# Performance work log

Measured on AMD Instinct MI355X. Metric: run time of the kernel, lower is better.

Reference implementation:

```python
import jax, jax.numpy as jnp
import numpy as np

HEADS = 4
DIM_HEAD = 32
NUM_GROUPS = 8
EPS = 1e-5


def setup_inputs() -> dict:
    key = jax.random.key(0)
    k1, k2, k3, k4 = jax.random.split(key, 4)
    dim = 256
    hidden = HEADS * DIM_HEAD  # 128
    x = jax.random.normal(k1, (4, dim, 64, 64), dtype=jnp.float32)
    # 1x1 convs stored as plain matrices [out_ch, in_ch]
    w_qkv = jax.random.normal(k2, (hidden * 3, dim), dtype=jnp.float32) * (1.0 / np.sqrt(dim))
    w_out = jax.random.normal(k3, (dim, hidden), dtype=jnp.float32) * (1.0 / np.sqrt(hidden))
    b_out = jnp.zeros((dim,), dtype=jnp.float32)
    gamma = jnp.ones((dim,), dtype=jnp.float32)
    beta = jnp.zeros((dim,), dtype=jnp.float32)
    return {"x": x, "w_qkv": w_qkv, "w_out": w_out, "b_out": b_out, "gamma": gamma, "beta": beta}


def group_norm(x, gamma, beta):
    b, c, h, w = x.shape
    xg = x.reshape(b, NUM_GROUPS, c // NUM_GROUPS, h, w)
    mean = xg.mean(axis=(2, 3, 4), keepdims=True)
    var = xg.var(axis=(2, 3, 4), keepdims=True)
    xg = (xg - mean) * jax.lax.rsqrt(var + EPS)
    x = xg.reshape(b, c, h, w)
    return x * gamma[None, :, None, None] + beta[None, :, None, None]


def reference(x, w_qkv, w_out, b_out, gamma, beta):
    b, c, h, w = x.shape
    n = h * w
    scale = DIM_HEAD ** -0.5
    xn = group_norm(x, gamma, beta)  # [b,c,h,w]
    # 1x1 conv QKV: [b, 3*hidden, n]
    qkv = jnp.einsum('oc,bchw->bohw', w_qkv, xn).reshape(b, 3 * HEADS * DIM_HEAD, n)
    q, k, v = jnp.split(qkv, 3, axis=1)
    # -> [b, heads, dim_head, n]
    q = q.reshape(b, HEADS, DIM_HEAD, n) * scale
    k = k.reshape(b, HEADS, DIM_HEAD, n)
    v = v.reshape(b, HEADS, DIM_HEAD, n)
    sim = jnp.einsum('bhdi,bhdj->bhij', q, k)  # [b,heads,n,n]
    sim = sim - jax.lax.stop_gradient(jnp.max(sim, axis=-1, keepdims=True))
    attn = jax.nn.softmax(sim, axis=-1)
    out = jnp.einsum('bhij,bhdj->bhid', attn, v)  # [b,heads,n,dim_head]
    # 'b h (x y) d -> b (h d) x y'
    out = out.transpose(0, 1, 3, 2).reshape(b, HEADS * DIM_HEAD, h, w)
    out = jnp.einsum('oc,bchw->bohw', w_out, out) + b_out[None, :, None, None]
    return out
```

## Files before the change

### kernel.cpp

```cpp
#include <hip/hip_runtime.h>
#include <hip/hip_bf16.h>

typedef float f32x4 __attribute__((ext_vector_type(4)));
typedef short s16x8 __attribute__((ext_vector_type(8)));

__device__ __forceinline__ short f2bf(float f){
  union { float f; unsigned u; } v; v.f = f;
  unsigned u = v.u;
  u += 0x7fffu + ((u >> 16) & 1u);
  return (short)(u >> 16);
}

__device__ __forceinline__ f32x4 mfma16(s16x8 a, s16x8 b, f32x4 c){
  return __builtin_amdgcn_mfma_f32_16x16x32_bf16(a, b, c, 0, 0, 0);
}

__device__ __forceinline__ float fexp2(float x){
#if __has_builtin(__builtin_amdgcn_exp2f)
  return __builtin_amdgcn_exp2f(x);
#else
  float r; asm("v_exp_f32 %0, %1" : "=v"(r) : "v"(x)); return r;
#endif
}

__device__ __forceinline__ unsigned cvtpk(float lo, float hi){
  unsigned r; asm("v_cvt_pk_bf16_f32 %0, %1, %2" : "=v"(r) : "v"(lo), "v"(hi));
  return r;
}

__global__ __launch_bounds__(256) void gn_stats_cvt_k(const float* __restrict__ x,
                                                      const float* __restrict__ wq,
                                                      const float* __restrict__ wo,
                                                      float* __restrict__ part,
                                                      short* __restrict__ wq_bf,
                                                      short* __restrict__ wo_bf){
  int bx = blockIdx.x;
  if (bx >= 1024){
    int i = (bx - 1024)*256 + threadIdx.x;
    if (i < 384*256) wq_bf[i] = f2bf(wq[i]);
    if (i < 256*128) wo_bf[i] = f2bf(wo[i]);
    return;
  }
  const float4* base = ((const float4*)x) + (size_t)bx * 1024;
  float s = 0.f, s2 = 0.f;
  #pragma unroll
  for (int i = threadIdx.x; i < 1024; i += 256){
    float4 v = base[i];
    s  += v.x + v.y + v.z + v.w;
    s2 += v.x*v.x + v.y*v.y + v.z*v.z + v.w*v.w;
  }
  #pragma unroll
  for (int off = 32; off; off >>= 1){ s += __shfl_down(s, off); s2 += __shfl_down(s2, off); }
  __shared__ float ls[8];
  int wid = threadIdx.x >> 6;
  if ((threadIdx.x & 63) == 0){ ls[wid] = s; ls[4 + wid] = s2; }
  __syncthreads();
  if (threadIdx.x == 0){
    part[bx*2]     = ls[0]+ls[1]+ls[2]+ls[3];
    part[bx*2 + 1] = ls[4]+ls[5]+ls[6]+ls[7];
  }
}

__global__ __launch_bounds__(256) void gn_apply_k(const float* __restrict__ x,
                                                  const float* __restrict__ gamma,
                                                  const float* __restrict__ beta,
                                                  const float* __restrict__ part,
                                                  short* __restrict__ xnt){
  __shared__ float lds[64][65];
  int b = blockIdx.z, cg = blockIdx.y, pt = blockIdx.x;
  int t = threadIdx.x;
  int ci = t >> 6, pj = t & 63;
  int p0 = pt * 64;
  float mean[2], rs[2];
  #pragma unroll
  for (int gi = 0; gi < 2; ++gi){
    int bg = b*8 + cg*2 + gi;
    float S = 0.f, S2 = 0.f;
    #pragma unroll
    for (int sl = 0; sl < 32; ++sl){ S += part[(bg*32+sl)*2]; S2 += part[(bg*32+sl)*2+1]; }
    float m = S * (1.f/131072.f);
    mean[gi] = m;
    rs[gi] = rsqrtf(S2 * (1.f/131072.f) - m*m + 1e-5f);
  }
  #pragma unroll
  for (int r = 0; r < 16; ++r){
    int cl = r*4 + ci;
    int c = cg*64 + cl;
    float v = x[((size_t)(b*256 + c))*4096 + p0 + pj];
    int gl = cl >> 5;
    v = (v - mean[gl]) * rs[gl] * gamma[c] + beta[c];
    lds[cl][pj] = v;
  }
  __syncthreads();
  #pragma unroll
  for (int r = 0; r < 16; ++r){
    int pl = r*4 + ci;
    int cl = pj;
    xnt[((size_t)(b*4096 + p0 + pl))*256 + cg*64 + cl] = f2bf(lds[cl][pl]);
  }
}

__global__ __launch_bounds__(256) void qkv_gemm_k(const short* __restrict__ wq_bf,
                                                  const short* __restrict__ xnt,
                                                  short* __restrict__ q,
                                                  short* __restrict__ k,
                                                  short* __restrict__ vt){
  int b = blockIdx.z;
  int obase = blockIdx.y * 64;
  int pbase = blockIdx.x * 64;
  int t = threadIdx.x;
  int w = t >> 6, l = t & 63;
  int l15 = l & 15, g = l >> 4;
  int orow = obase + w*16 + l15;
  const s16x8* wrow = (const s16x8*)(wq_bf + (size_t)orow * 256);
  s16x8 af[8];
  #pragma unroll
  for (int kk = 0; kk < 8; ++kk) af[kk] = wrow[kk*4 + g];
  const float QSC = 0.17677669529663687f * 1.4426950408889634f;
  #pragma unroll
  for (int pt = 0; pt < 4; ++pt){
    int p = pbase + pt*16 + l15;
    const s16x8* xr = (const s16x8*)(xnt + ((size_t)b*4096 + p) * 256);
    f32x4 acc = {0.f,0.f,0.f,0.f};
    #pragma unroll
    for (int kk = 0; kk < 8; ++kk) acc = mfma16(af[kk], xr[kk*4 + g], acc);
    int pp = p & 31;
    int pos = ((pp>>2)&3)*8 + ((pp>>4)&1)*4 + (pp&3);
    int pperm = (p & ~31) | pos;
    #pragma unroll
    for (int e = 0; e < 4; ++e){
      int og = obase + w*16 + 4*g + e;
      float v = acc[e];
      int sec = og >> 7;
      int oh = og & 127;
      int h = oh >> 5, d = oh & 31;
      size_t qk_idx = (((size_t)b*4 + h)*4096 + p)*32 + d;
      if (sec == 0)      q[qk_idx] = f2bf(v * QSC);
      else if (sec == 1) k[qk_idx] = f2bf(v);
      else vt[(((size_t)b*4 + h)*32 + d)*4096 + pperm] = f2bf(v);
    }
  }
}

__global__ __launch_bounds__(256, 4) void flash_k(const short* __restrict__ q,
                                                  const short* __restrict__ k,
                                                  const short* __restrict__ vt,
                                                  short* __restrict__ at){
  __shared__ short ldsS[4*4096];
  __shared__ float sums[4][64];
  int bid = blockIdx.x;
  int lin = (bid & 7)*128 + (bid >> 3);
  int bh = lin >> 6;
  int rt  = lin & 63;
  int b = bh >> 2, h = bh & 3;
  int blkrow = rt * 64;
  int t = threadIdx.x;
  int w = t >> 6, l = t & 63, l15 = l & 15, g = l >> 4;

  const short* qb = q  + (size_t)bh * 4096 * 32;
  const short* kb = k  + (size_t)bh * 4096 * 32;
  const short* vb = vt + (size_t)bh * 32 * 4096;

  s16x8 qf[4];
  #pragma unroll
  for (int it = 0; it < 4; ++it)
    qf[it] = *(const s16x8*)(qb + (size_t)(blkrow + it*16 + l15)*32 + 8*g);

  int wbase = w * 4096;
  int rk = wbase + l15*40 + g*8;
  int rv = wbase + 1280 + l15*40 + g*8;
  int row = l >> 1, hi = (l & 1) * 16;
  int wk = wbase + row*40 + hi;
  int wv = wbase + 1280 + row*40 + hi;

  const short* kq = kb + (size_t)w*32768 + l*16;
  const short* vq = vb + (size_t)row*4096 + w*1024 + hi;

  f32x4 o[4][2];
  float lsum[4];
  #pragma unroll
  for (int it = 0; it < 4; ++it){
    o[it][0] = (f32x4){0.f,0.f,0.f,0.f};
    o[it][1] = (f32x4){0.f,0.f,0.f,0.f};
    lsum[it] = 0.f;
  }
  const f32x4 zero = {0.f,0.f,0.f,0.f};

  s16x8 ka0, ka1, va0, va1;

#define FENCE() asm volatile("" ::: "memory")
#define KVLOAD() do{ ka0 = *(const s16x8*)kq; ka1 = *(const s16x8*)(kq + 8); kq += 1024; \
                     va0 = *(const s16x8*)vq; va1 = *(const s16x8*)(vq + 8); vq += 32; }while(0)
#define KVSTORE() do{ *(s16x8*)&ldsS[wk] = ka0; *(s16x8*)&ldsS[wk + 8] = ka1; \
                      *(s16x8*)&ldsS[wv] = va0; *(s16x8*)&ldsS[wv + 8] = va1; }while(0)
#define COMPUTE() do{ \
    s16x8 kf0 = *(const s16x8*)&ldsS[rk]; \
    s16x8 kf1 = *(const s16x8*)&ldsS[rk + 640]; \
    s16x8 vf0 = *(const s16x8*)&ldsS[rv]; \
    s16x8 vf1 = *(const s16x8*)&ldsS[rv + 640]; \
    _Pragma("unroll") \
    for (int it = 0; it < 4; ++it){ \
      f32x4 s0 = mfma16(kf0, qf[it], zero); \
      f32x4 s1 = mfma16(kf1, qf[it], zero); \
      float p0=fexp2(s0[0]), p1=fexp2(s0[1]), p2=fexp2(s0[2]), p3=fexp2(s0[3]); \
      float p4=fexp2(s1[0]), p5=fexp2(s1[1]), p6=fexp2(s1[2]), p7=fexp2(s1[3]); \
      lsum[it] += ((p0+p1)+(p2+p3)) + ((p4+p5)+(p6+p7)); \
      union { s16x8 v; unsigned u[4]; } pf; \
      pf.u[0] = cvtpk(p0,p1); pf.u[1] = cvtpk(p2,p3); \
      pf.u[2] = cvtpk(p4,p5); pf.u[3] = cvtpk(p6,p7); \
      o[it][0] = mfma16(pf.v, vf0, o[it][0]); \
      o[it][1] = mfma16(pf.v, vf1, o[it][1]); \
    } \
  }while(0)

  KVLOAD();
  KVSTORE();
  FENCE();
  for (int tt = 0; tt < 31; ++tt){
    KVLOAD();
    COMPUTE();
    FENCE();
    KVSTORE();
    FENCE();
  }
  COMPUTE();
#undef KVLOAD
#undef KVSTORE
#undef COMPUTE

  #pragma unroll
  for (int it = 0; it < 4; ++it){
    lsum[it] += __shfl_xor(lsum[it], 16);
    lsum[it] += __shfl_xor(lsum[it], 32);
  }

  FENCE();
  float* cmb = (float*)ldsS;
  #pragma unroll
  for (int it = 0; it < 4; ++it){
    #pragma unroll
    for (int e = 0; e < 4; ++e){
      int r = it*16 + 4*g + e;
      cmb[w*2048 + r*32 + l15]      = o[it][0][e];
      cmb[w*2048 + r*32 + 16 + l15] = o[it][1][e];
    }
    if (l < 16) sums[w][it*16 + l15] = lsum[it];
  }
  __syncthreads();

  int r = t >> 2, d0 = (t & 3) * 8;
  float den = (sums[0][r] + sums[1][r]) + (sums[2][r] + sums[3][r]);
  float inv = 1.f / den;
  s16x8 outv;
  #pragma unroll
  for (int kk = 0; kk < 8; ++kk){
    float num = (cmb[r*32 + d0 + kk] + cmb[2048 + r*32 + d0 + kk])
              + (cmb[4096 + r*32 + d0 + kk] + cmb[6144 + r*32 + d0 + kk]);
    outv[kk] = f2bf(num * inv);
  }
  *(s16x8*)(at + ((size_t)b*4096 + blkrow + r)*128 + h*32 + d0) = outv;
}

__global__ __launch_bounds__(256) void out_gemm_k(const short* __restrict__ wo_bf,
                                                  const short* __restrict__ at,
                                                  const float* __restrict__ b_out,
                                                  float* __restrict__ out){
  int b = blockIdx.z;
  int obase = blockIdx.y * 64;
  int pbase = blockIdx.x * 64;
  int t = threadIdx.x, w = t >> 6, l = t & 63, l15 = l & 15, g = l >> 4;
  int orow = obase + w*16 + l15;
  const s16x8* wrow = (const s16x8*)(wo_bf + (size_t)orow * 128);
  s16x8 af[4];
  #pragma unroll
  for (int kk = 0; kk < 4; ++kk) af[kk] = wrow[kk*4 + g];
  #pragma unroll
  for (int pt = 0; pt < 4; ++pt){
    int p = pbase + pt*16 + l15;
    const s16x8* xr = (const s16x8*)(at + ((size_t)b*4096 + p) * 128);
    f32x4 acc = {0.f,0.f,0.f,0.f};
    #pragma unroll
    for (int kk = 0; kk < 4; ++kk) acc = mfma16(af[kk], xr[kk*4 + g], acc);
    #pragma unroll
    for (int e = 0; e < 4; ++e){
      int og = obase + w*16 + 4*g + e;
      out[((size_t)b*256 + og)*4096 + p] = acc[e] + b_out[og];
    }
  }
}

extern "C" void kernel_launch(void* const* d_in, const int* in_sizes, int n_in,
                              void* d_out, int out_size, void* d_ws, size_t ws_size,
                              hipStream_t stream){
  const float* x     = (const float*)d_in[0];
  const float* w_qkv = (const float*)d_in[1];
  const float* w_out = (const float*)d_in[2];
  const float* b_out = (const float*)d_in[3];
  const float* gamma = (const float*)d_in[4];
  const float* beta  = (const float*)d_in[5];
  float* out = (float*)d_out;

  char* ws = (char*)d_ws;
  short* wq_bf = (short*)(ws);
  short* wo_bf = (short*)(ws + 196608);
  short* xnt   = (short*)(ws + 264192);
  short* qbuf  = (short*)(ws + 8652800);
  short* kbuf  = (short*)(ws + 12847104);
  short* vtbuf = (short*)(ws + 17041408);
  short* atbuf = (short*)(ws + 21235712);
  float* part  = (float*)(ws + 21235712);

  hipLaunchKernelGGL(gn_stats_cvt_k, dim3(1408), dim3(256), 0, stream, x, w_qkv, w_out, part, wq_bf, wo_bf);
  hipLaunchKernelGGL(gn_apply_k, dim3(64,4,4),   dim3(256), 0, stream, x, gamma, beta, part, xnt);
  hipLaunchKernelGGL(qkv_gemm_k, dim3(64,6,4),   dim3(256), 0, stream, wq_bf, xnt, qbuf, kbuf, vtbuf);
  hipLaunchKernelGGL(flash_k,    dim3(1024),     dim3(256), 0, stream, qbuf, kbuf, vtbuf, atbuf);
  hipLaunchKernelGGL(out_gemm_k, dim3(64,4,4),   dim3(256), 0, stream, wo_bf, atbuf, b_out, out);
}
```

Before: 110.4 us.

## Fuse group-norm apply into QKV GEMM and slim flash epilogue LDS usage

Merges the group-norm apply kernel with the QKV projection. Each block normalizes a 32-pixel tile of all 256 channels into LDS as bf16 and then runs the MFMA GEMM for all 384 output rows. This removes the xnt intermediate write and read to global memory and drops one kernel launch. The flash epilogue now combines per-wave partial outputs in two half-passes, each wave using its own padded LDS region, which drops the separate sums array. The fused kernel has only 512 blocks, makes narrower 32-float strided reads of x, and reloads weight fragments per output tile.

```diff
diff --git a/kernel.cpp b/kernel.cpp
--- a/kernel.cpp
+++ b/kernel.cpp
@@ -61,83 +61,84 @@
   }
 }
 
-__global__ __launch_bounds__(256) void gn_apply_k(const float* __restrict__ x,
-                                                  const float* __restrict__ gamma,
-                                                  const float* __restrict__ beta,
-                                                  const float* __restrict__ part,
-                                                  short* __restrict__ xnt){
-  __shared__ float lds[64][65];
-  int b = blockIdx.z, cg = blockIdx.y, pt = blockIdx.x;
+__global__ __launch_bounds__(256) void gn_qkv_k(const float* __restrict__ x,
+                                                const float* __restrict__ part,
+                                                const float* __restrict__ gamma,
+                                                const float* __restrict__ beta,
+                                                const short* __restrict__ wq_bf,
+                                                short* __restrict__ q,
+                                                short* __restrict__ k,
+                                                short* __restrict__ vt){
+  __shared__ float stg[64][33];
+  __shared__ short xl[32*264];
+  __shared__ float mstat[16];
+  int b = blockIdx.y;
+  int p0 = blockIdx.x * 32;
   int t = threadIdx.x;
-  int ci = t >> 6, pj = t & 63;
-  int p0 = pt * 64;
-  float mean[2], rs[2];
-  #pragma unroll
-  for (int gi = 0; gi < 2; ++gi){
-    int bg = b*8 + cg*2 + gi;
-    float S = 0.f, S2 = 0.f;
-    #pragma unroll
-    for (int sl = 0; sl < 32; ++sl){ S += part[(bg*32+sl)*2]; S2 += part[(bg*32+sl)*2+1]; }
-    float m = S * (1.f/131072.f);
-    mean[gi] = m;
-    rs[gi] = rsqrtf(S2 * (1.f/131072.f) - m*m + 1e-5f);
-  }
-  #pragma unroll
-  for (int r = 0; r < 16; ++r){
-    int cl = r*4 + ci;
-    int c = cg*64 + cl;
-    float v = x[((size_t)(b*256 + c))*4096 + p0 + pj];
-    int gl = cl >> 5;
-    v = (v - mean[gl]) * rs[gl] * gamma[c] + beta[c];
-    lds[cl][pj] = v;
-  }
-  __syncthreads();
-  #pragma unroll
-  for (int r = 0; r < 16; ++r){
-    int pl = r*4 + ci;
-    int cl = pj;
-    xnt[((size_t)(b*4096 + p0 + pl))*256 + cg*64 + cl] = f2bf(lds[cl][pl]);
-  }
-}
-
-__global__ __launch_bounds__(256) void qkv_gemm_k(const short* __restrict__ wq_bf,
-                                                  const short* __restrict__ xnt,
-                                                  short* __restrict__ q,
-                                                  short* __restrict__ k,
-                                                  short* __restrict__ vt){
-  int b = blockIdx.z;
-  int obase = blockIdx.y * 64;
-  int pbase = blockIdx.x * 64;
-  int t = threadIdx.x;
-  int w = t >> 6, l = t & 63;
-  int l15 = l & 15, g = l >> 4;
-  int orow = obase + w*16 + l15;
-  const s16x8* wrow = (const s16x8*)(wq_bf + (size_t)orow * 256);
-  s16x8 af[8];
-  #pragma unroll
-  for (int kk = 0; kk < 8; ++kk) af[kk] = wrow[kk*4 + g];
+  {
+    int gi = t >> 5, sl = t & 31;
+    float S  = part[((b*8+gi)*32 + sl)*2];
+    float S2 = part[((b*8+gi)*32 + sl)*2 + 1];
+    #pragma unroll
+    for (int m = 16; m; m >>= 1){ S += __shfl_xor(S, m); S2 += __shfl_xor(S2, m); }
+    if (sl == 0){
+      float mn = S * (1.f/131072.f);
+      mstat[gi]   = mn;
+      mstat[8+gi] = rsqrtf(S2 * (1.f/131072.f) - mn*mn + 1e-5f);
+    }
+  }
+  __syncthreads();
+  int pj = t & 31, ci8 = t >> 5;
+  for (int cc = 0; cc < 4; ++cc){
+    #pragma unroll
+    for (int r = 0; r < 8; ++r){
+      int cl = r*8 + ci8;
+      int c = cc*64 + cl;
+      float v = x[((size_t)(b*256 + c))*4096 + p0 + pj];
+      int gl = c >> 5;
+      v = (v - mstat[gl]) * mstat[8+gl] * gamma[c] + beta[c];
+      stg[cl][pj] = v;
+    }
+    __syncthreads();
+    {
+      s16x8 pack;
+      #pragma unroll
+      for (int i = 0; i < 8; ++i) pack[i] = f2bf(stg[ci8*8 + i][pj]);
+      *(s16x8*)&xl[pj*264 + cc*64 + ci8*8] = pack;
+    }
+    __syncthreads();
+  }
+  int w = t >> 6, l = t & 63, l15 = l & 15, g = l >> 4;
   const float QSC = 0.17677669529663687f * 1.4426950408889634f;
   #pragma unroll
-  for (int pt = 0; pt < 4; ++pt){
-    int p = pbase + pt*16 + l15;
-    const s16x8* xr = (const s16x8*)(xnt + ((size_t)b*4096 + p) * 256);
-    f32x4 acc = {0.f,0.f,0.f,0.f};
-    #pragma unroll
-    for (int kk = 0; kk < 8; ++kk) acc = mfma16(af[kk], xr[kk*4 + g], acc);
-    int pp = p & 31;
-    int pos = ((pp>>2)&3)*8 + ((pp>>4)&1)*4 + (pp&3);
-    int pperm = (p & ~31) | pos;
-    #pragma unroll
-    for (int e = 0; e < 4; ++e){
-      int og = obase + w*16 + 4*g + e;
-      float v = acc[e];
-      int sec = og >> 7;
-      int oh = og & 127;
-      int h = oh >> 5, d = oh & 31;
-      size_t qk_idx = (((size_t)b*4 + h)*4096 + p)*32 + d;
-      if (sec == 0)      q[qk_idx] = f2bf(v * QSC);
-      else if (sec == 1) k[qk_idx] = f2bf(v);
-      else vt[(((size_t)b*4 + h)*32 + d)*4096 + pperm] = f2bf(v);
+  for (int ot = 0; ot < 6; ++ot){
+    int orow = w*96 + ot*16 + l15;
+    const s16x8* wrow = (const s16x8*)(wq_bf + (size_t)orow * 256);
+    s16x8 af[8];
+    #pragma unroll
+    for (int kk = 0; kk < 8; ++kk) af[kk] = wrow[kk*4 + g];
+    #pragma unroll
+    for (int pt = 0; pt < 2; ++pt){
+      f32x4 acc = {0.f,0.f,0.f,0.f};
+      #pragma unroll
+      for (int kk = 0; kk < 8; ++kk)
+        acc = mfma16(af[kk], *(const s16x8*)&xl[(pt*16+l15)*264 + kk*32 + g*8], acc);
+      int p = p0 + pt*16 + l15;
+      int pp = p & 31;
+      int pos = ((pp>>2)&3)*8 + ((pp>>4)&1)*4 + (pp&3);
+      int pperm = (p & ~31) | pos;
+      #pragma unroll
+      for (int e = 0; e < 4; ++e){
+        int og = w*96 + ot*16 + 4*g + e;
+        float v = acc[e];
+        int sec = og >> 7;
+        int oh = og & 127;
+        int h = oh >> 5, d = oh & 31;
+        size_t qk_idx = (((size_t)b*4 + h)*4096 + p)*32 + d;
+        if (sec == 0)      q[qk_idx] = f2bf(v * QSC);
+        else if (sec == 1) k[qk_idx] = f2bf(v);
+        else vt[(((size_t)b*4 + h)*32 + d)*4096 + pperm] = f2bf(v);
+      }
     }
   }
 }
@@ -147,7 +148,6 @@
                                                   const short* __restrict__ vt,
                                                   short* __restrict__ at){
   __shared__ short ldsS[4*4096];
-  __shared__ float sums[4][64];
   int bid = blockIdx.x;
   int lin = (bid & 7)*128 + (bid >> 3);
   int bh = lin >> 6;
@@ -235,30 +235,53 @@
   }
 
   FENCE();
-  float* cmb = (float*)ldsS;
+  float* cw = (float*)&ldsS[wbase];
   #pragma unroll
   for (int it = 0; it < 4; ++it){
     #pragma unroll
     for (int e = 0; e < 4; ++e){
       int r = it*16 + 4*g + e;
-      cmb[w*2048 + r*32 + l15]      = o[it][0][e];
-      cmb[w*2048 + r*32 + 16 + l15] = o[it][1][e];
-    }
-    if (l < 16) sums[w][it*16 + l15] = lsum[it];
-  }
-  __syncthreads();
-
-  int r = t >> 2, d0 = (t & 3) * 8;
-  float den = (sums[0][r] + sums[1][r]) + (sums[2][r] + sums[3][r]);
+      cw[r*17 + l15] = o[it][0][e];
+    }
+    if (l < 16) cw[1088 + it*16 + l15] = lsum[it];
+  }
+  __syncthreads();
+  int rr = t >> 2, a = t & 3;
+  size_t rowbase = ((size_t)b*4096 + blkrow + rr)*128 + h*32;
+  float den = 0.f, n0 = 0.f, n1 = 0.f, n2 = 0.f, n3 = 0.f;
+  #pragma unroll
+  for (int w2 = 0; w2 < 4; ++w2){
+    const float* cr = (const float*)&ldsS[w2*4096];
+    den += cr[1088 + rr];
+    n0 += cr[rr*17 + a*4];
+    n1 += cr[rr*17 + a*4 + 1];
+    n2 += cr[rr*17 + a*4 + 2];
+    n3 += cr[rr*17 + a*4 + 3];
+  }
   float inv = 1.f / den;
-  s16x8 outv;
-  #pragma unroll
-  for (int kk = 0; kk < 8; ++kk){
-    float num = (cmb[r*32 + d0 + kk] + cmb[2048 + r*32 + d0 + kk])
-              + (cmb[4096 + r*32 + d0 + kk] + cmb[6144 + r*32 + d0 + kk]);
-    outv[kk] = f2bf(num * inv);
-  }
-  *(s16x8*)(at + ((size_t)b*4096 + blkrow + r)*128 + h*32 + d0) = outv;
+  { uint2 u; u.x = cvtpk(n0*inv, n1*inv); u.y = cvtpk(n2*inv, n3*inv);
+    *(uint2*)(at + rowbase + a*4) = u; }
+  __syncthreads();
+  #pragma unroll
+  for (int it = 0; it < 4; ++it){
+    #pragma unroll
+    for (int e = 0; e < 4; ++e){
+      int r = it*16 + 4*g + e;
+      cw[r*17 + l15] = o[it][1][e];
+    }
+  }
+  __syncthreads();
+  n0 = 0.f; n1 = 0.f; n2 = 0.f; n3 = 0.f;
+  #pragma unroll
+  for (int w2 = 0; w2 < 4; ++w2){
+    const float* cr = (const float*)&ldsS[w2*4096];
+    n0 += cr[rr*17 + a*4];
+    n1 += cr[rr*17 + a*4 + 1];
+    n2 += cr[rr*17 + a*4 + 2];
+    n3 += cr[rr*17 + a*4 + 3];
+  }
+  { uint2 u; u.x = cvtpk(n0*inv, n1*inv); u.y = cvtpk(n2*inv, n3*inv);
+    *(uint2*)(at + rowbase + 16 + a*4) = u; }
 }
 
 __global__ __launch_bounds__(256) void out_gemm_k(const short* __restrict__ wo_bf,
@@ -303,16 +326,14 @@
   char* ws = (char*)d_ws;
   short* wq_bf = (short*)(ws);
   short* wo_bf = (short*)(ws + 196608);
-  short* xnt   = (short*)(ws + 264192);
   short* qbuf  = (short*)(ws + 8652800);
   short* kbuf  = (short*)(ws + 12847104);
   short* vtbuf = (short*)(ws + 17041408);
   short* atbuf = (short*)(ws + 21235712);
   float* part  = (float*)(ws + 21235712);
 
-  hipLaunchKernelGGL(gn_stats_cvt_k, dim3(1408), dim3(256), 0, stream, x, w_qkv, w_out, part, wq_bf, wo_bf);
-  hipLaunchKernelGGL(gn_apply_k, dim3(64,4,4),   dim3(256), 0, stream, x, gamma, beta, part, xnt);
-  hipLaunchKernelGGL(qkv_gemm_k, dim3(64,6,4),   dim3(256), 0, stream, wq_bf, xnt, qbuf, kbuf, vtbuf);
-  hipLaunchKernelGGL(flash_k,    dim3(1024),     dim3(256), 0, stream, qbuf, kbuf, vtbuf, atbuf);
-  hipLaunchKernelGGL(out_gemm_k, dim3(64,4,4),   dim3(256), 0, stream, wo_bf, atbuf, b_out, out);
-}
+  hipLaunchKernelGGL(gn_stats_cvt_k, dim3(1408),    dim3(256), 0, stream, x, w_qkv, w_out, part, wq_bf, wo_bf);
+  hipLaunchKernelGGL(gn_qkv_k,       dim3(128,4),   dim3(256), 0, stream, x, part, gamma, beta, wq_bf, qbuf, kbuf, vtbuf);
+  hipLaunchKernelGGL(flash_k,        dim3(1024),    dim3(256), 0, stream, qbuf, kbuf, vtbuf, atbuf);
+  hipLaunchKernelGGL(out_gemm_k,     dim3(64,4,4),  dim3(256), 0, stream, wo_bf, atbuf, b_out, out);
+}
```

Measured after the change: 91.65 us. -17.0%, faster.
